# Performance work log

Measured on AMD Instinct MI355X. Metric: run time of the kernel, lower is better.

## Reference

```python
import jax, jax.numpy as jnp
import numpy as np


def setup_inputs() -> dict:
    key = jax.random.key(0)
    x = jax.random.normal(key, (8192, 512), dtype=jnp.float32)
    return {"x": x}


def reference(x):
    n = x.shape[0]
    sq = jnp.sum(x * x, axis=1)                      # [N] squared L2 norms
    # pairwise squared distances: ||xi||^2 + ||xj||^2 - 2 xi.xj
    dist = -2.0 * (x @ x.T) + sq[None, :] + sq[:, None]  # [N, N]
    mask = jnp.triu(jnp.ones((n, n), dtype=bool), k=1)   # strict upper triangle
    # torch: norm = max row L2 norm, detached (.data)
    norm = jax.lax.stop_gradient(jnp.sqrt(jnp.max(sq)))
    count = n * (n - 1) // 2
    loss = jnp.sum(jnp.where(mask, dist, 0.0)) / (norm * count)
    return loss
```

## Files before the change

kernel.cpp:

```cpp
#include <hip/hip_runtime.h>


#define NROWS 8192
#define NCOLS 512
#define NB1   256
#define PS    (NB1 * NCOLS)
#define PM    (PS + NB1)

__global__ __launch_bounds__(256) void ndl_pass1(const float* __restrict__ x,
                                                 float* __restrict__ ws) {
    __shared__ float colsum[NCOLS];
    __shared__ float s_part[4];
    __shared__ float m_part[4];
    const int t    = threadIdx.x;
    const int lane = t & 63;
    const int wave = t >> 6;

    colsum[t]       = 0.f;
    colsum[t + 256] = 0.f;
    __syncthreads();

    const int row0 = blockIdx.x * 32 + wave * 8;
    const float4* xv = (const float4*)x;

    float col[8] = {0.f, 0.f, 0.f, 0.f, 0.f, 0.f, 0.f, 0.f};
    float sp = 0.f;
    float maxsq = 0.f;

    #pragma unroll
    for (int r = 0; r < 8; ++r) {
        const int row = row0 + r;
        float4 a = xv[row * 128 + lane * 2];
        float4 b = xv[row * 128 + lane * 2 + 1];
        col[0] += a.x; col[1] += a.y; col[2] += a.z; col[3] += a.w;
        col[4] += b.x; col[5] += b.y; col[6] += b.z; col[7] += b.w;
        float rsq = a.x*a.x + a.y*a.y + a.z*a.z + a.w*a.w
                  + b.x*b.x + b.y*b.y + b.z*b.z + b.w*b.w;
        sp += rsq;
        #pragma unroll
        for (int off = 1; off < 64; off <<= 1)
            rsq += __shfl_xor(rsq, off, 64);
        maxsq = fmaxf(maxsq, rsq);
    }

    const int base = lane * 8;
    #pragma unroll
    for (int k = 0; k < 8; ++k)
        atomicAdd(&colsum[base + k], col[k]);

    #pragma unroll
    for (int off = 1; off < 64; off <<= 1)
        sp += __shfl_xor(sp, off, 64);
    if (lane == 0) { s_part[wave] = sp; m_part[wave] = maxsq; }
    __syncthreads();

    float* o = ws + (size_t)blockIdx.x * NCOLS;
    o[t]       = colsum[t];
    o[t + 256] = colsum[t + 256];
    if (t == 0) {
        ws[PS + blockIdx.x] = s_part[0] + s_part[1] + s_part[2] + s_part[3];
        ws[PM + blockIdx.x] = fmaxf(fmaxf(m_part[0], m_part[1]),
                                    fmaxf(m_part[2], m_part[3]));
    }
}

__global__ __launch_bounds__(1024) void ndl_pass2(const float* __restrict__ ws,
                                                  float* __restrict__ out) {
    __shared__ float cs[1024];
    __shared__ float red_q[16];
    __shared__ float red_s[16];
    __shared__ float red_m[16];
    const int t    = threadIdx.x;
    const int lane = t & 63;
    const int wave = t >> 6;
    const int col  = t & 511;
    const int half = t >> 9;

    const float* p = ws + (size_t)(half * 128) * NCOLS + col;
    float acc = 0.f;
    #pragma unroll 8
    for (int i = 0; i < 128; ++i)
        acc += p[(size_t)i * NCOLS];
    cs[t] = acc;
    __syncthreads();

    float qv = 0.f;
    if (t < 512) {
        float c = cs[t] + cs[t + 512];
        qv = c * c;
    }
    float sv = (t < NB1) ? ws[PS + t] : 0.f;
    float mv = (t < NB1) ? ws[PM + t] : 0.f;

    #pragma unroll
    for (int off = 1; off < 64; off <<= 1) {
        qv += __shfl_xor(qv, off, 64);
        sv += __shfl_xor(sv, off, 64);
        mv  = fmaxf(mv, __shfl_xor(mv, off, 64));
    }
    if (lane == 0) { red_q[wave] = qv; red_s[wave] = sv; red_m[wave] = mv; }
    __syncthreads();

    if (t == 0) {
        double ss = 0.0, S = 0.0;
        float  mx = 0.f;
        #pragma unroll
        for (int w = 0; w < 16; ++w) {
            ss += (double)red_q[w];
            S  += (double)red_s[w];
            mx  = fmaxf(mx, red_m[w]);
        }
        double numer = (double)NROWS * S - ss;
        double count = (double)NROWS * ((double)NROWS - 1.0) * 0.5;
        out[0] = (float)(numer / (sqrt((double)mx) * count));
    }
}

extern "C" void kernel_launch(void* const* d_in, const int* in_sizes, int n_in,
                              void* d_out, int out_size, void* d_ws, size_t ws_size,
                              hipStream_t stream) {
    const float* x = (const float*)d_in[0];
    float* out = (float*)d_out;
    float* ws  = (float*)d_ws;

    ndl_pass1<<<NB1, 256, 0, stream>>>(x, ws);
    ndl_pass2<<<1, 1024, 0, stream>>>(ws, out);
}
```

Before: 73.21 us.

## Split single-block column reduction into multi-block pass plus tiny final reduce

The second-stage reduction of per-block column sums used to run in one 1024-thread block that read the whole 256x512 partial buffer serially. It is now split into a 64-block kernel, where each block reduces 8 columns and squares them and also combines the row-sum and max partials, followed by a 64-thread kernel for the final combine. The aim is to spread a latency-bound serial read across many compute units. In exchange it adds a third kernel launch, and each block reads columns in narrow 8-float (32-byte) pieces, which coalesces poorly.

```diff
diff --git a/kernel.cpp b/kernel.cpp
--- a/kernel.cpp
+++ b/kernel.cpp
@@ -4,8 +4,12 @@
 #define NROWS 8192
 #define NCOLS 512
 #define NB1   256
+#define NB2   64
 #define PS    (NB1 * NCOLS)
 #define PM    (PS + NB1)
+#define PQ    (PM + NB1)
+#define PS2   (PQ + NB2)
+#define PM2   (PS2 + NB2)
 
 __global__ __launch_bounds__(256) void ndl_pass1(const float* __restrict__ x,
                                                  float* __restrict__ ws) {
@@ -64,55 +68,64 @@
     }
 }
 
-__global__ __launch_bounds__(1024) void ndl_pass2(const float* __restrict__ ws,
-                                                  float* __restrict__ out) {
-    __shared__ float cs[1024];
-    __shared__ float red_q[16];
-    __shared__ float red_s[16];
-    __shared__ float red_m[16];
+__global__ __launch_bounds__(256) void ndl_pass2a(const float* __restrict__ ws_in,
+                                                  float* __restrict__ ws) {
+    __shared__ float wred[4 * 8];
     const int t    = threadIdx.x;
     const int lane = t & 63;
     const int wave = t >> 6;
-    const int col  = t & 511;
-    const int half = t >> 9;
+    const int j    = blockIdx.x;
+    const int c    = j * 8 + (t & 7);
+    const int i    = t >> 3;
 
-    const float* p = ws + (size_t)(half * 128) * NCOLS + col;
+    const float* p = ws_in + (size_t)(i * 8) * NCOLS + c;
     float acc = 0.f;
-    #pragma unroll 8
-    for (int i = 0; i < 128; ++i)
-        acc += p[(size_t)i * NCOLS];
-    cs[t] = acc;
+    #pragma unroll
+    for (int k = 0; k < 8; ++k)
+        acc += p[(size_t)k * NCOLS];
+
+    acc += __shfl_xor(acc, 8, 64);
+    acc += __shfl_xor(acc, 16, 64);
+    acc += __shfl_xor(acc, 32, 64);
+    if (lane < 8) wred[wave * 8 + lane] = acc;
     __syncthreads();
 
-    float qv = 0.f;
-    if (t < 512) {
-        float c = cs[t] + cs[t + 512];
-        qv = c * c;
+    if (t < 8) {
+        float cs = wred[t] + wred[8 + t] + wred[16 + t] + wred[24 + t];
+        float q  = cs * cs;
+        q += __shfl_xor(q, 1, 64);
+        q += __shfl_xor(q, 2, 64);
+        q += __shfl_xor(q, 4, 64);
+        if (t == 0) ws[PQ + j] = q;
     }
-    float sv = (t < NB1) ? ws[PS + t] : 0.f;
-    float mv = (t < NB1) ? ws[PM + t] : 0.f;
+    if (t == 0) {
+        float s = 0.f, m = 0.f;
+        #pragma unroll
+        for (int k = 0; k < 4; ++k) {
+            s += ws_in[PS + j * 4 + k];
+            m  = fmaxf(m, ws_in[PM + j * 4 + k]);
+        }
+        ws[PS2 + j] = s;
+        ws[PM2 + j] = m;
+    }
+}
 
+__global__ __launch_bounds__(64) void ndl_pass2b(const float* __restrict__ ws,
+                                                 float* __restrict__ out) {
+    const int t = threadIdx.x;
+    float qv = ws[PQ + t];
+    float sv = ws[PS2 + t];
+    float mv = ws[PM2 + t];
     #pragma unroll
     for (int off = 1; off < 64; off <<= 1) {
         qv += __shfl_xor(qv, off, 64);
         sv += __shfl_xor(sv, off, 64);
         mv  = fmaxf(mv, __shfl_xor(mv, off, 64));
     }
-    if (lane == 0) { red_q[wave] = qv; red_s[wave] = sv; red_m[wave] = mv; }
-    __syncthreads();
-
     if (t == 0) {
-        double ss = 0.0, S = 0.0;
-        float  mx = 0.f;
-        #pragma unroll
-        for (int w = 0; w < 16; ++w) {
-            ss += (double)red_q[w];
-            S  += (double)red_s[w];
-            mx  = fmaxf(mx, red_m[w]);
-        }
-        double numer = (double)NROWS * S - ss;
+        double numer = (double)NROWS * (double)sv - (double)qv;
         double count = (double)NROWS * ((double)NROWS - 1.0) * 0.5;
-        out[0] = (float)(numer / (sqrt((double)mx) * count));
+        out[0] = (float)(numer / (sqrt((double)mv) * count));
     }
 }
 
@@ -124,5 +137,6 @@
     float* ws  = (float*)d_ws;
 
     ndl_pass1<<<NB1, 256, 0, stream>>>(x, ws);
-    ndl_pass2<<<1, 1024, 0, stream>>>(ws, out);
+    ndl_pass2a<<<NB2, 256, 0, stream>>>(ws, ws);
+    ndl_pass2b<<<1, 64, 0, stream>>>(ws, out);
 }
```

Result: faster. 68.01 us (-7.1%).
